# Performance work log

Hardware: AMD Instinct MI355X
Metric: run time of the kernel (lower is better)

The kernel has to match this reference:

```python
import jax, jax.numpy as jnp
import numpy as np

NUM_SEQS = 32
KV_LEN = 2048          # cached context length per sequence
NUM_HEADS = 16
HEAD_SIZE = 128
SCALE = 0.08838834764831845  # 1/sqrt(HEAD_SIZE)
TOTAL_SLOTS = NUM_SEQS * KV_LEN


def setup_inputs() -> dict:
    key = jax.random.key(0)
    kq, kk, kv, kc = jax.random.split(key, 4)
    q = jax.random.normal(kq, (NUM_SEQS, NUM_HEADS, HEAD_SIZE), dtype=jnp.float32)
    k = jax.random.normal(kk, (NUM_SEQS, NUM_HEADS, HEAD_SIZE), dtype=jnp.float32)
    v = jax.random.normal(kv, (NUM_SEQS, NUM_HEADS, HEAD_SIZE), dtype=jnp.float32)
    kv_cache = jax.random.normal(kc, (2, TOTAL_SLOTS, NUM_HEADS, HEAD_SIZE), dtype=jnp.float32)
    # each sequence owns slots [i*KV_LEN, (i+1)*KV_LEN); new token written at the last slot
    slot_mapping = jnp.arange(NUM_SEQS, dtype=jnp.int64) * KV_LEN + (KV_LEN - 1)
    return {"q": q, "k": k, "v": v, "kv_cache": kv_cache, "slot_mapping": slot_mapping}


def reference(q, k, v, kv_cache, slot_mapping):
    # 1) reshape_and_cache: scatter new k/v into the paged cache at slot_mapping
    kv_cache = kv_cache.at[0, slot_mapping].set(k)
    kv_cache = kv_cache.at[1, slot_mapping].set(v)
    # 2) paged attention decode: each query attends over its own contiguous slot range
    keys = kv_cache[0].reshape(NUM_SEQS, KV_LEN, NUM_HEADS, HEAD_SIZE)
    vals = kv_cache[1].reshape(NUM_SEQS, KV_LEN, NUM_HEADS, HEAD_SIZE)
    scores = jnp.einsum("shd,sthd->sht", q, keys) * SCALE  # [seqs, heads, kv_len]
    probs = jax.nn.softmax(scores, axis=-1)
    out = jnp.einsum("sht,sthd->shd", probs, vals)         # [seqs, heads, head_size]
    return out
```

## Files before the change

kernel.cpp:

```cpp
#include <hip/hip_runtime.h>

constexpr int NUM_SEQS  = 32;
constexpr int KV_LEN    = 2048;
constexpr int NUM_HEADS = 16;
constexpr int HEAD_SIZE = 128;
constexpr float SCALE   = 0.08838834764831845f;

constexpr int HSTRIDE = NUM_HEADS * HEAD_SIZE;
constexpr size_t KV_PLANE = (size_t)NUM_SEQS * KV_LEN * HSTRIDE;

constexpr int NPART   = 4;
constexpr int PSTRIDE = HEAD_SIZE + 2;

template <int NP>
__global__ __launch_bounds__(256, 8)
void paged_decode_partial(const float* __restrict__ q,
                          const float* __restrict__ knew,
                          const float* __restrict__ vnew,
                          const float* __restrict__ kv,
                          const int*  __restrict__ slot_map,
                          float* __restrict__ ws,
                          float* __restrict__ out)
{
    constexpr int CH = KV_LEN / NP;

    const int bid = blockIdx.x;
    const int c   = bid & (NP - 1);
    const int sh  = bid / NP;
    const int s   = sh >> 4;
    const int h   = sh & (NUM_HEADS - 1);

    const int tid  = threadIdx.x;
    const int half = tid >> 5;
    const int lane = tid & 31;

    __shared__ float sc[CH];
    __shared__ float red[4];
    __shared__ float part[8][HEAD_SIZE];

    const int qoff = sh * HEAD_SIZE;
    const float* kbase = kv + (size_t)s * KV_LEN * HSTRIDE + (size_t)h * HEAD_SIZE;
    const float* vbase = kbase + KV_PLANE;
    const int t_new = slot_map[s] - s * KV_LEN;
    const int tbeg  = c * CH;

    const float4 qv = *reinterpret_cast<const float4*>(q + qoff + lane * 4);

    for (int base = 0; base < CH; base += 32) {
        const int l0 = base + half * 4;
        const int t0 = tbeg + l0;

        const float* p0 = (t0 + 0 == t_new) ? (knew + qoff) : (kbase + (size_t)(t0 + 0) * HSTRIDE);
        const float* p1 = (t0 + 1 == t_new) ? (knew + qoff) : (kbase + (size_t)(t0 + 1) * HSTRIDE);
        const float* p2 = (t0 + 2 == t_new) ? (knew + qoff) : (kbase + (size_t)(t0 + 2) * HSTRIDE);
        const float* p3 = (t0 + 3 == t_new) ? (knew + qoff) : (kbase + (size_t)(t0 + 3) * HSTRIDE);

        const float4 k0 = *reinterpret_cast<const float4*>(p0 + lane * 4);
        const float4 k1 = *reinterpret_cast<const float4*>(p1 + lane * 4);
        const float4 k2 = *reinterpret_cast<const float4*>(p2 + lane * 4);
        const float4 k3 = *reinterpret_cast<const float4*>(p3 + lane * 4);

        float d0 = fmaf(k0.x, qv.x, fmaf(k0.y, qv.y, fmaf(k0.z, qv.z, k0.w * qv.w)));
        float d1 = fmaf(k1.x, qv.x, fmaf(k1.y, qv.y, fmaf(k1.z, qv.z, k1.w * qv.w)));
        float d2 = fmaf(k2.x, qv.x, fmaf(k2.y, qv.y, fmaf(k2.z, qv.z, k2.w * qv.w)));
        float d3 = fmaf(k3.x, qv.x, fmaf(k3.y, qv.y, fmaf(k3.z, qv.z, k3.w * qv.w)));

        #pragma unroll
        for (int off = 16; off > 0; off >>= 1) {
            d0 += __shfl_xor(d0, off);
            d1 += __shfl_xor(d1, off);
            d2 += __shfl_xor(d2, off);
            d3 += __shfl_xor(d3, off);
        }
        if (lane == 0) {
            sc[l0 + 0] = d0 * SCALE;
            sc[l0 + 1] = d1 * SCALE;
            sc[l0 + 2] = d2 * SCALE;
            sc[l0 + 3] = d3 * SCALE;
        }
    }
    __syncthreads();

    float m = -1e30f;
    #pragma unroll
    for (int t = tid; t < CH; t += 256) m = fmaxf(m, sc[t]);
    #pragma unroll
    for (int off = 32; off > 0; off >>= 1) m = fmaxf(m, __shfl_xor(m, off));
    if ((tid & 63) == 0) red[tid >> 6] = m;
    __syncthreads();
    const float mblk = fmaxf(fmaxf(red[0], red[1]), fmaxf(red[2], red[3]));

    float lsum = 0.f;
    #pragma unroll
    for (int t = tid; t < CH; t += 256) {
        const float e = __expf(sc[t] - mblk);
        sc[t] = e;
        lsum += e;
    }
    #pragma unroll
    for (int off = 32; off > 0; off >>= 1) lsum += __shfl_xor(lsum, off);
    __syncthreads();
    if ((tid & 63) == 0) red[tid >> 6] = lsum;
    __syncthreads();
    const float lloc = red[0] + red[1] + red[2] + red[3];

    float4 acc = make_float4(0.f, 0.f, 0.f, 0.f);
    for (int base = 0; base < CH; base += 32) {
        const int l0 = base + half * 4;
        const int t0 = tbeg + l0;

        const float* p0 = (t0 + 0 == t_new) ? (vnew + qoff) : (vbase + (size_t)(t0 + 0) * HSTRIDE);
        const float* p1 = (t0 + 1 == t_new) ? (vnew + qoff) : (vbase + (size_t)(t0 + 1) * HSTRIDE);
        const float* p2 = (t0 + 2 == t_new) ? (vnew + qoff) : (vbase + (size_t)(t0 + 2) * HSTRIDE);
        const float* p3 = (t0 + 3 == t_new) ? (vnew + qoff) : (vbase + (size_t)(t0 + 3) * HSTRIDE);

        const float4 v0 = *reinterpret_cast<const float4*>(p0 + lane * 4);
        const float4 v1 = *reinterpret_cast<const float4*>(p1 + lane * 4);
        const float4 v2 = *reinterpret_cast<const float4*>(p2 + lane * 4);
        const float4 v3 = *reinterpret_cast<const float4*>(p3 + lane * 4);

        const float w0 = sc[l0 + 0];
        const float w1 = sc[l0 + 1];
        const float w2 = sc[l0 + 2];
        const float w3 = sc[l0 + 3];

        acc.x = fmaf(w0, v0.x, acc.x); acc.y = fmaf(w0, v0.y, acc.y);
        acc.z = fmaf(w0, v0.z, acc.z); acc.w = fmaf(w0, v0.w, acc.w);
        acc.x = fmaf(w1, v1.x, acc.x); acc.y = fmaf(w1, v1.y, acc.y);
        acc.z = fmaf(w1, v1.z, acc.z); acc.w = fmaf(w1, v1.w, acc.w);
        acc.x = fmaf(w2, v2.x, acc.x); acc.y = fmaf(w2, v2.y, acc.y);
        acc.z = fmaf(w2, v2.z, acc.z); acc.w = fmaf(w2, v2.w, acc.w);
        acc.x = fmaf(w3, v3.x, acc.x); acc.y = fmaf(w3, v3.y, acc.y);
        acc.z = fmaf(w3, v3.z, acc.z); acc.w = fmaf(w3, v3.w, acc.w);
    }

    *reinterpret_cast<float4*>(&part[half][lane * 4]) = acc;
    __syncthreads();

    if constexpr (NP == 1) {
        if (tid < HEAD_SIZE) {
            float o = 0.f;
            #pragma unroll
            for (int i = 0; i < 8; ++i) o += part[i][tid];
            out[qoff + tid] = o / lloc;
        }
    } else {
        float* rec = ws + (size_t)bid * PSTRIDE;
        if (tid < HEAD_SIZE) {
            float o = 0.f;
            #pragma unroll
            for (int i = 0; i < 8; ++i) o += part[i][tid];
            rec[2 + tid] = o;
        }
        if (tid == 0) {
            rec[0] = mblk;
            rec[1] = lloc;
        }
    }
}

__global__ __launch_bounds__(128)
void paged_decode_reduce(const float* __restrict__ ws, float* __restrict__ out)
{
    const int sh = blockIdx.x;
    const int i  = threadIdx.x;
    const float* rec0 = ws + (size_t)sh * NPART * PSTRIDE;

    float M = -1e30f;
    #pragma unroll
    for (int c = 0; c < NPART; ++c) M = fmaxf(M, rec0[c * PSTRIDE]);

    float L = 0.f, o = 0.f;
    #pragma unroll
    for (int c = 0; c < NPART; ++c) {
        const float w = __expf(rec0[c * PSTRIDE] - M);
        L = fmaf(rec0[c * PSTRIDE + 1], w, L);
        o = fmaf(rec0[c * PSTRIDE + 2 + i], w, o);
    }
    out[sh * HEAD_SIZE + i] = o / L;
}

extern "C" void kernel_launch(void* const* d_in, const int* in_sizes, int n_in,
                              void* d_out, int out_size, void* d_ws, size_t ws_size,
                              hipStream_t stream) {
    const float* q    = (const float*)d_in[0];
    const float* k    = (const float*)d_in[1];
    const float* v    = (const float*)d_in[2];
    const float* kv   = (const float*)d_in[3];
    const int*   slot = (const int*)d_in[4];
    float* out = (float*)d_out;

    const size_t need = (size_t)NUM_SEQS * NUM_HEADS * NPART * PSTRIDE * sizeof(float);
    if (d_ws != nullptr && ws_size >= need) {
        dim3 grid1(NUM_SEQS * NUM_HEADS * NPART);
        hipLaunchKernelGGL(paged_decode_partial<NPART>, grid1, dim3(256), 0, stream,
                           q, k, v, kv, slot, (float*)d_ws, out);
        dim3 grid2(NUM_SEQS * NUM_HEADS);
        hipLaunchKernelGGL(paged_decode_reduce, grid2, dim3(128), 0, stream,
                           (float*)d_ws, out);
    } else {
        dim3 grid(NUM_SEQS * NUM_HEADS);
        hipLaunchKernelGGL(paged_decode_partial<1>, grid, dim3(256), 0, stream,
                           q, k, v, kv, slot, nullptr, out);
    }
}
```

Measured before the change: 1.299 ms.

## Fuse K and V passes into single-pass online softmax with register prefetch

Replaces the two-pass scheme (scores into shared memory, softmax, then a second sweep over V) with a single pass in which each 32-lane group keeps a running max, sum and accumulator, loading K and V together and prefetching the next tile into registers. The per-group partial states are merged through shared memory at the end. Block indexing is reordered so that adjacent blocks cover different heads of the same sequence chunk, and launch bounds drop from 8 to 4 blocks per CU to leave room for the extra prefetch registers. The intent is to cut the intermediate syncs and the serialised second memory sweep, at the cost of more exp work and higher register pressure.

```diff
diff --git a/kernel.cpp b/kernel.cpp
--- a/kernel.cpp
+++ b/kernel.cpp
@@ -13,57 +13,54 @@
 constexpr int PSTRIDE = HEAD_SIZE + 2;
 
 template <int NP>
-__global__ __launch_bounds__(256, 8)
-void paged_decode_partial(const float* __restrict__ q,
-                          const float* __restrict__ knew,
-                          const float* __restrict__ vnew,
-                          const float* __restrict__ kv,
-                          const int*  __restrict__ slot_map,
-                          float* __restrict__ ws,
-                          float* __restrict__ out)
+__global__ __launch_bounds__(256, 4)
+void fd_kernel(const float* __restrict__ q,
+               const float* __restrict__ knew,
+               const float* __restrict__ vnew,
+               const float* __restrict__ kv,
+               const int*  __restrict__ slot_map,
+               float* __restrict__ ws,
+               float* __restrict__ out)
 {
-    constexpr int CH = KV_LEN / NP;
+    constexpr int CH  = KV_LEN / NP;
+    constexpr int NIT = CH / 32;
 
     const int bid = blockIdx.x;
-    const int c   = bid & (NP - 1);
-    const int sh  = bid / NP;
-    const int s   = sh >> 4;
-    const int h   = sh & (NUM_HEADS - 1);
+    const int h   = bid & (NUM_HEADS - 1);
+    const int scv = bid >> 4;
+    const int c   = scv & (NP - 1);
+    const int s   = scv / NP;
+    const int sh  = s * NUM_HEADS + h;
 
     const int tid  = threadIdx.x;
     const int half = tid >> 5;
     const int lane = tid & 31;
 
-    __shared__ float sc[CH];
-    __shared__ float red[4];
-    __shared__ float part[8][HEAD_SIZE];
-
     const int qoff = sh * HEAD_SIZE;
     const float* kbase = kv + (size_t)s * KV_LEN * HSTRIDE + (size_t)h * HEAD_SIZE;
     const float* vbase = kbase + KV_PLANE;
     const int t_new = slot_map[s] - s * KV_LEN;
-    const int tbeg  = c * CH;
 
-    const float4 qv = *reinterpret_cast<const float4*>(q + qoff + lane * 4);
+    float4 qv = *reinterpret_cast<const float4*>(q + qoff + lane * 4);
+    qv.x *= SCALE; qv.y *= SCALE; qv.z *= SCALE; qv.w *= SCALE;
 
-    for (int base = 0; base < CH; base += 32) {
-        const int l0 = base + half * 4;
-        const int t0 = tbeg + l0;
+    float  m   = -1e30f;
+    float  l   = 0.f;
+    float4 acc = make_float4(0.f, 0.f, 0.f, 0.f);
 
-        const float* p0 = (t0 + 0 == t_new) ? (knew + qoff) : (kbase + (size_t)(t0 + 0) * HSTRIDE);
-        const float* p1 = (t0 + 1 == t_new) ? (knew + qoff) : (kbase + (size_t)(t0 + 1) * HSTRIDE);
-        const float* p2 = (t0 + 2 == t_new) ? (knew + qoff) : (kbase + (size_t)(t0 + 2) * HSTRIDE);
-        const float* p3 = (t0 + 3 == t_new) ? (knew + qoff) : (kbase + (size_t)(t0 + 3) * HSTRIDE);
+    auto kptr = [&](int t) {
+        return ((t == t_new) ? (knew + qoff) : (kbase + (size_t)t * HSTRIDE)) + lane * 4;
+    };
+    auto vptr = [&](int t) {
+        return ((t == t_new) ? (vnew + qoff) : (vbase + (size_t)t * HSTRIDE)) + lane * 4;
+    };
 
-        const float4 k0 = *reinterpret_cast<const float4*>(p0 + lane * 4);
-        const float4 k1 = *reinterpret_cast<const float4*>(p1 + lane * 4);
-        const float4 k2 = *reinterpret_cast<const float4*>(p2 + lane * 4);
-        const float4 k3 = *reinterpret_cast<const float4*>(p3 + lane * 4);
-
-        float d0 = fmaf(k0.x, qv.x, fmaf(k0.y, qv.y, fmaf(k0.z, qv.z, k0.w * qv.w)));
-        float d1 = fmaf(k1.x, qv.x, fmaf(k1.y, qv.y, fmaf(k1.z, qv.z, k1.w * qv.w)));
-        float d2 = fmaf(k2.x, qv.x, fmaf(k2.y, qv.y, fmaf(k2.z, qv.z, k2.w * qv.w)));
-        float d3 = fmaf(k3.x, qv.x, fmaf(k3.y, qv.y, fmaf(k3.z, qv.z, k3.w * qv.w)));
+    auto compute = [&](const float4& K0, const float4& K1, const float4& K2, const float4& K3,
+                       const float4& V0, const float4& V1, const float4& V2, const float4& V3) {
+        float d0 = fmaf(K0.x, qv.x, fmaf(K0.y, qv.y, fmaf(K0.z, qv.z, K0.w * qv.w)));
+        float d1 = fmaf(K1.x, qv.x, fmaf(K1.y, qv.y, fmaf(K1.z, qv.z, K1.w * qv.w)));
+        float d2 = fmaf(K2.x, qv.x, fmaf(K2.y, qv.y, fmaf(K2.z, qv.z, K2.w * qv.w)));
+        float d3 = fmaf(K3.x, qv.x, fmaf(K3.y, qv.y, fmaf(K3.z, qv.z, K3.w * qv.w)));
 
         #pragma unroll
         for (int off = 16; off > 0; off >>= 1) {
@@ -72,95 +69,83 @@
             d2 += __shfl_xor(d2, off);
             d3 += __shfl_xor(d3, off);
         }
-        if (lane == 0) {
-            sc[l0 + 0] = d0 * SCALE;
-            sc[l0 + 1] = d1 * SCALE;
-            sc[l0 + 2] = d2 * SCALE;
-            sc[l0 + 3] = d3 * SCALE;
-        }
+
+        const float mn  = fmaxf(fmaxf(m, fmaxf(d0, d1)), fmaxf(d2, d3));
+        const float scl = __expf(m - mn);
+        const float e0  = __expf(d0 - mn);
+        const float e1  = __expf(d1 - mn);
+        const float e2  = __expf(d2 - mn);
+        const float e3  = __expf(d3 - mn);
+        m = mn;
+        l = fmaf(l, scl, (e0 + e1) + (e2 + e3));
+
+        acc.x = fmaf(e0, V0.x, fmaf(e1, V1.x, fmaf(e2, V2.x, fmaf(e3, V3.x, acc.x * scl))));
+        acc.y = fmaf(e0, V0.y, fmaf(e1, V1.y, fmaf(e2, V2.y, fmaf(e3, V3.y, acc.y * scl))));
+        acc.z = fmaf(e0, V0.z, fmaf(e1, V1.z, fmaf(e2, V2.z, fmaf(e3, V3.z, acc.z * scl))));
+        acc.w = fmaf(e0, V0.w, fmaf(e1, V1.w, fmaf(e2, V2.w, fmaf(e3, V3.w, acc.w * scl))));
+    };
+
+    int t0 = c * CH + half * 4;
+
+    float4 kc0 = *reinterpret_cast<const float4*>(kptr(t0 + 0));
+    float4 kc1 = *reinterpret_cast<const float4*>(kptr(t0 + 1));
+    float4 kc2 = *reinterpret_cast<const float4*>(kptr(t0 + 2));
+    float4 kc3 = *reinterpret_cast<const float4*>(kptr(t0 + 3));
+    float4 vc0 = *reinterpret_cast<const float4*>(vptr(t0 + 0));
+    float4 vc1 = *reinterpret_cast<const float4*>(vptr(t0 + 1));
+    float4 vc2 = *reinterpret_cast<const float4*>(vptr(t0 + 2));
+    float4 vc3 = *reinterpret_cast<const float4*>(vptr(t0 + 3));
+
+    for (int it = 0; it < NIT - 1; ++it) {
+        const int tn = t0 + 32;
+        float4 kn0 = *reinterpret_cast<const float4*>(kptr(tn + 0));
+        float4 kn1 = *reinterpret_cast<const float4*>(kptr(tn + 1));
+        float4 kn2 = *reinterpret_cast<const float4*>(kptr(tn + 2));
+        float4 kn3 = *reinterpret_cast<const float4*>(kptr(tn + 3));
+        float4 vn0 = *reinterpret_cast<const float4*>(vptr(tn + 0));
+        float4 vn1 = *reinterpret_cast<const float4*>(vptr(tn + 1));
+        float4 vn2 = *reinterpret_cast<const float4*>(vptr(tn + 2));
+        float4 vn3 = *reinterpret_cast<const float4*>(vptr(tn + 3));
+
+        compute(kc0, kc1, kc2, kc3, vc0, vc1, vc2, vc3);
+
+        kc0 = kn0; kc1 = kn1; kc2 = kn2; kc3 = kn3;
+        vc0 = vn0; vc1 = vn1; vc2 = vn2; vc3 = vn3;
+        t0 = tn;
     }
+    compute(kc0, kc1, kc2, kc3, vc0, vc1, vc2, vc3);
+
+    __shared__ float sm[8];
+    __shared__ float sl[8];
+    __shared__ float part[8][HEAD_SIZE];
+
+    *reinterpret_cast<float4*>(&part[half][lane * 4]) = acc;
+    if (lane == 0) { sm[half] = m; sl[half] = l; }
     __syncthreads();
 
-    float m = -1e30f;
-    #pragma unroll
-    for (int t = tid; t < CH; t += 256) m = fmaxf(m, sc[t]);
-    #pragma unroll
-    for (int off = 32; off > 0; off >>= 1) m = fmaxf(m, __shfl_xor(m, off));
-    if ((tid & 63) == 0) red[tid >> 6] = m;
-    __syncthreads();
-    const float mblk = fmaxf(fmaxf(red[0], red[1]), fmaxf(red[2], red[3]));
-
-    float lsum = 0.f;
-    #pragma unroll
-    for (int t = tid; t < CH; t += 256) {
-        const float e = __expf(sc[t] - mblk);
-        sc[t] = e;
-        lsum += e;
-    }
-    #pragma unroll
-    for (int off = 32; off > 0; off >>= 1) lsum += __shfl_xor(lsum, off);
-    __syncthreads();
-    if ((tid & 63) == 0) red[tid >> 6] = lsum;
-    __syncthreads();
-    const float lloc = red[0] + red[1] + red[2] + red[3];
-
-    float4 acc = make_float4(0.f, 0.f, 0.f, 0.f);
-    for (int base = 0; base < CH; base += 32) {
-        const int l0 = base + half * 4;
-        const int t0 = tbeg + l0;
-
-        const float* p0 = (t0 + 0 == t_new) ? (vnew + qoff) : (vbase + (size_t)(t0 + 0) * HSTRIDE);
-        const float* p1 = (t0 + 1 == t_new) ? (vnew + qoff) : (vbase + (size_t)(t0 + 1) * HSTRIDE);
-        const float* p2 = (t0 + 2 == t_new) ? (vnew + qoff) : (vbase + (size_t)(t0 + 2) * HSTRIDE);
-        const float* p3 = (t0 + 3 == t_new) ? (vnew + qoff) : (vbase + (size_t)(t0 + 3) * HSTRIDE);
-
-        const float4 v0 = *reinterpret_cast<const float4*>(p0 + lane * 4);
-        const float4 v1 = *reinterpret_cast<const float4*>(p1 + lane * 4);
-        const float4 v2 = *reinterpret_cast<const float4*>(p2 + lane * 4);
-        const float4 v3 = *reinterpret_cast<const float4*>(p3 + lane * 4);
-
-        const float w0 = sc[l0 + 0];
-        const float w1 = sc[l0 + 1];
-        const float w2 = sc[l0 + 2];
-        const float w3 = sc[l0 + 3];
-
-        acc.x = fmaf(w0, v0.x, acc.x); acc.y = fmaf(w0, v0.y, acc.y);
-        acc.z = fmaf(w0, v0.z, acc.z); acc.w = fmaf(w0, v0.w, acc.w);
-        acc.x = fmaf(w1, v1.x, acc.x); acc.y = fmaf(w1, v1.y, acc.y);
-        acc.z = fmaf(w1, v1.z, acc.z); acc.w = fmaf(w1, v1.w, acc.w);
-        acc.x = fmaf(w2, v2.x, acc.x); acc.y = fmaf(w2, v2.y, acc.y);
-        acc.z = fmaf(w2, v2.z, acc.z); acc.w = fmaf(w2, v2.w, acc.w);
-        acc.x = fmaf(w3, v3.x, acc.x); acc.y = fmaf(w3, v3.y, acc.y);
-        acc.z = fmaf(w3, v3.z, acc.z); acc.w = fmaf(w3, v3.w, acc.w);
-    }
-
-    *reinterpret_cast<float4*>(&part[half][lane * 4]) = acc;
-    __syncthreads();
-
-    if constexpr (NP == 1) {
-        if (tid < HEAD_SIZE) {
-            float o = 0.f;
-            #pragma unroll
-            for (int i = 0; i < 8; ++i) o += part[i][tid];
-            out[qoff + tid] = o / lloc;
+    if (tid < HEAD_SIZE) {
+        float M = sm[0];
+        #pragma unroll
+        for (int i = 1; i < 8; ++i) M = fmaxf(M, sm[i]);
+        float L = 0.f, o = 0.f;
+        #pragma unroll
+        for (int i = 0; i < 8; ++i) {
+            const float w = __expf(sm[i] - M);
+            L = fmaf(sl[i], w, L);
+            o = fmaf(part[i][tid], w, o);
         }
-    } else {
-        float* rec = ws + (size_t)bid * PSTRIDE;
-        if (tid < HEAD_SIZE) {
-            float o = 0.f;
-            #pragma unroll
-            for (int i = 0; i < 8; ++i) o += part[i][tid];
+        if constexpr (NP == 1) {
+            out[qoff + tid] = o / L;
+        } else {
+            float* rec = ws + (size_t)(sh * NP + c) * PSTRIDE;
             rec[2 + tid] = o;
-        }
-        if (tid == 0) {
-            rec[0] = mblk;
-            rec[1] = lloc;
+            if (tid == 0) { rec[0] = M; rec[1] = L; }
         }
     }
 }
 
 __global__ __launch_bounds__(128)
-void paged_decode_reduce(const float* __restrict__ ws, float* __restrict__ out)
+void fd_reduce(const float* __restrict__ ws, float* __restrict__ out)
 {
     const int sh = blockIdx.x;
     const int i  = threadIdx.x;
@@ -193,14 +178,14 @@
     const size_t need = (size_t)NUM_SEQS * NUM_HEADS * NPART * PSTRIDE * sizeof(float);
     if (d_ws != nullptr && ws_size >= need) {
         dim3 grid1(NUM_SEQS * NUM_HEADS * NPART);
-        hipLaunchKernelGGL(paged_decode_partial<NPART>, grid1, dim3(256), 0, stream,
+        hipLaunchKernelGGL(fd_kernel<NPART>, grid1, dim3(256), 0, stream,
                            q, k, v, kv, slot, (float*)d_ws, out);
         dim3 grid2(NUM_SEQS * NUM_HEADS);
-        hipLaunchKernelGGL(paged_decode_reduce, grid2, dim3(128), 0, stream,
+        hipLaunchKernelGGL(fd_reduce, grid2, dim3(128), 0, stream,
                            (float*)d_ws, out);
     } else {
         dim3 grid(NUM_SEQS * NUM_HEADS);
-        hipLaunchKernelGGL(paged_decode_partial<1>, grid, dim3(256), 0, stream,
+        hipLaunchKernelGGL(fd_kernel<1>, grid, dim3(256), 0, stream,
                            q, k, v, kv, slot, nullptr, out);
     }
 }
```

Measured after the change: 1.300 ms. Within noise of the previous version (+0.1%).
